# Kernel optimization log

Hardware: AMD Instinct MI355X
Metric: run time of the kernel (lower is better)

Reference implementation:

```python
import jax, jax.numpy as jnp
import numpy as np

B, N, D, H, DG = 1, 1024, 512, 8, 64
DK = D // H
EPS = 1e-5


def _layer_norm(x, g, b):
    m = jnp.mean(x, axis=-1, keepdims=True)
    v = jnp.var(x, axis=-1, keepdims=True)
    return (x - m) / jnp.sqrt(v + EPS) * g + b


def _box_rel_embedding(box):
    # box: (B, N, 4) = x_min, y_min, x_max, y_max
    x_min, y_min, x_max, y_max = [box[..., i] for i in range(4)]  # each (B, N)
    cx = (x_min + x_max) * 0.5
    cy = (y_min + y_max) * 0.5
    w = x_max - x_min + 1.0
    h = y_max - y_min + 1.0
    dx = jnp.log(jnp.clip(jnp.abs((cx[:, :, None] - cx[:, None, :]) / w[:, :, None]), 0.001))
    dy = jnp.log(jnp.clip(jnp.abs((cy[:, :, None] - cy[:, None, :]) / h[:, :, None]), 0.001))
    dw = jnp.log(w[:, :, None] / w[:, None, :])
    dh = jnp.log(h[:, :, None] / h[:, None, :])
    pos = jnp.stack([dx, dy, dw, dh], axis=-1)  # (B, N, N, 4)
    dim_mat = 1.0 / jnp.power(1000.0, jnp.arange(DG // 8, dtype=jnp.float32) / (DG // 8))  # (8,)
    mul = (100.0 * pos[..., None] * dim_mat).reshape(pos.shape[0], pos.shape[1], pos.shape[2], -1)  # (B,N,N,32)
    return jnp.concatenate([jnp.sin(mul), jnp.cos(mul)], axis=-1)  # (B, N, N, 64)


def _split_heads(x, W, b):
    # torch permute(2,0,1,3).view(-1, len, d_k): head-major flattening
    return (x @ W.T + b).reshape(B, N, H, DK).transpose(2, 0, 1, 3).reshape(H * B, N, DK)


def _forward(input_query, input_key, input_value, input_box,
             Wq, bq, Wk, bk, Wv, bv, Wo, bo, WG_w, WG_b,
             ln0_g, ln0_b, ln_g, ln_b):
    residual = input_query
    emb = _box_rel_embedding(input_box)  # (B, N, N, 64)
    # per-head linear (64 -> 1) then relu: (B, H, N, N)
    w_g = jax.nn.relu(jnp.einsum('bijg,hg->bhij', emb, WG_w) + WG_b[None, :, None, None])
    q = _split_heads(input_query, Wq, bq)  # (H*B, N, DK)
    k = _split_heads(input_key, Wk, bk)
    v = _split_heads(input_value, Wv, bv)
    scores = jnp.einsum('xnd,xmd->xnm', q, k) / np.sqrt(DK).astype(np.float32)  # (H*B, N, N)
    # original adds (B,H,N,N) to (H*B,N,N): only valid for B==1
    w_mn = jax.nn.softmax(jnp.log(jnp.clip(w_g.reshape(H * B, N, N), 1e-6)) + scores, axis=-1)
    x = jnp.einsum('xnm,xmd->xnd', w_mn, v)  # (H*B, N, DK)
    # faithful to original: transpose(1,2) then view(nbatches, -1, h*d_k)
    x = x.transpose(0, 2, 1).reshape(B, -1, H * DK)  # (B, N, D)
    out0 = _layer_norm(x + residual, ln0_g, ln0_b)
    out = out0 @ Wo.T + bo  # dropout = identity (eval mode)
    return _layer_norm(out + out0, ln_g, ln_b)


def setup_inputs() -> dict:
    key = jax.random.key(0)
    ks = jax.random.split(key, 12)
    inp = {}
    inp['input_query'] = jax.random.normal(ks[0], (B, N, D), dtype=jnp.float32)
    inp['input_key'] = jax.random.normal(ks[1], (B, N, D), dtype=jnp.float32)
    inp['input_value'] = jax.random.normal(ks[2], (B, N, D), dtype=jnp.float32)
    mins = jax.random.uniform(ks[3], (B, N, 2), dtype=jnp.float32) * 500.0
    sizes = jax.random.uniform(ks[4], (B, N, 2), dtype=jnp.float32) * 99.0 + 1.0
    inp['input_box'] = jnp.concatenate([mins, mins + sizes], axis=-1)  # valid boxes
    s = 0.02
    inp['Wq'] = jax.random.normal(ks[5], (D, D), dtype=jnp.float32) * s
    inp['bq'] = jnp.zeros((D,), dtype=jnp.float32)
    inp['Wk'] = jax.random.normal(ks[6], (D, D), dtype=jnp.float32) * s
    inp['bk'] = jnp.zeros((D,), dtype=jnp.float32)
    inp['Wv'] = jax.random.normal(ks[7], (D, D), dtype=jnp.float32) * s
    inp['bv'] = jnp.zeros((D,), dtype=jnp.float32)
    inp['Wo'] = jax.random.normal(ks[8], (D, D), dtype=jnp.float32) * s
    inp['bo'] = jnp.zeros((D,), dtype=jnp.float32)
    inp['WG_w'] = jax.random.normal(ks[9], (H, DG), dtype=jnp.float32) * 0.1
    inp['WG_b'] = jax.random.normal(ks[10], (H,), dtype=jnp.float32) * 0.1
    inp['ln0_g'] = jnp.ones((D,), dtype=jnp.float32)
    inp['ln0_b'] = jnp.zeros((D,), dtype=jnp.float32)
    inp['ln_g'] = jnp.ones((D,), dtype=jnp.float32)
    inp['ln_b'] = jnp.zeros((D,), dtype=jnp.float32)
    return inp


def reference(input_query, input_key, input_value, input_box,
              Wq, bq, Wk, bk, Wv, bv, Wo, bo, WG_w, WG_b,
              ln0_g, ln0_b, ln_g, ln_b):
    return _forward(input_query, input_key, input_value, input_box,
                    Wq, bq, Wk, bk, Wv, bv, Wo, bo, WG_w, WG_b,
                    ln0_g, ln0_b, ln_g, ln_b)
```

## Files before the change

kernel.cpp:

```cpp
#include <hip/hip_runtime.h>
#include <cstddef>

#define NTOK 1024
#define DMODEL 512
#define NHEAD 8
#define DKH 64
#define NSPLIT 8
#define JQ 128

typedef __attribute__((ext_vector_type(4))) float f32x4;
typedef __attribute__((ext_vector_type(8))) __bf16 bf16x8;
typedef __attribute__((ext_vector_type(4))) __bf16 bf16x4;
typedef __attribute__((ext_vector_type(4))) unsigned short u16x4;
typedef __attribute__((ext_vector_type(8))) unsigned short u16x8;
typedef __attribute__((ext_vector_type(4))) _Float16 f16x4;
typedef unsigned short ushort_t;

__device__ __forceinline__ float wave_sum_f(float v){
  #pragma unroll
  for (int m=1; m<64; m<<=1) v += __shfl_xor(v, m, 64);
  return v;
}
__device__ __forceinline__ unsigned short f2bf(float f){
  __bf16 b = (__bf16)f;
  return __builtin_bit_cast(unsigned short, b);
}
__device__ __forceinline__ float bf2f(unsigned short u){
  return (float)__builtin_bit_cast(__bf16, u);
}

__device__ __forceinline__ float fract_hw(float x){
  float r; asm("v_fract_f32 %0, %1" : "=v"(r) : "v"(x)); return r;
}
__device__ __forceinline__ float sin_rev(float rev){
  float f = fract_hw(rev);
  float s; asm("v_sin_f32 %0, %1" : "=v"(s) : "v"(f)); return s;
}
__device__ __forceinline__ float cos_rev(float rev){
  float f = fract_hw(rev);
  float c; asm("v_cos_f32 %0, %1" : "=v"(c) : "v"(f)); return c;
}
__device__ __forceinline__ float log_hw(float x){
  float l; asm("v_log_f32 %0, %1" : "=v"(l) : "v"(x));
  return 0.69314718056f * l;
}
__device__ __forceinline__ float exp_hw(float x){
  float y = x * 1.44269504f;
  float e; asm("v_exp_f32 %0, %1" : "=v"(e) : "v"(y));
  return e;
}

__global__ __launch_bounds__(256) void k_pre(
    const float* __restrict__ box, const float* __restrict__ WGw, const float* __restrict__ WGb,
    _Float16* __restrict__ wg16,
    const float* __restrict__ q, const float* __restrict__ k, const float* __restrict__ v,
    const float* __restrict__ wq, const float* __restrict__ wk, const float* __restrict__ wv,
    const float* __restrict__ wo,
    ushort_t* __restrict__ qb, ushort_t* __restrict__ kb, ushort_t* __restrict__ vb,
    ushort_t* __restrict__ wqb, ushort_t* __restrict__ wkb, ushort_t* __restrict__ wvb,
    ushort_t* __restrict__ wob){
  const int t = threadIdx.x;
  if (blockIdx.x >= 1024){
    int gi = (blockIdx.x - 1024)*256 + t;
    const float* s; ushort_t* d; int off;
    if (gi < 196608){
      int seg = gi >> 16;
      off = (gi & 65535)*8;
      s = seg==0 ? q : seg==1 ? k : v;
      d = seg==0 ? qb : seg==1 ? kb : vb;
    } else {
      int g2 = gi - 196608;
      int seg = g2 >> 15;
      off = (g2 & 32767)*8;
      s = seg==0 ? wq : seg==1 ? wk : seg==2 ? wv : wo;
      d = seg==0 ? wqb : seg==1 ? wkb : seg==2 ? wvb : wob;
    }
    float4 a = *(const float4*)(s + off);
    float4 b = *(const float4*)(s + off + 4);
    u16x4 o0, o1;
    o0[0]=f2bf(a.x); o0[1]=f2bf(a.y); o0[2]=f2bf(a.z); o0[3]=f2bf(a.w);
    o1[0]=f2bf(b.x); o1[1]=f2bf(b.y); o1[2]=f2bf(b.z); o1[3]=f2bf(b.w);
    *(u16x4*)(d + off) = o0;
    *(u16x4*)(d + off + 4) = o1;
    return;
  }
  __shared__ float arr[4][1024];
  #pragma unroll
  for (int u=0; u<4; u++){
    int idx = u*256 + t;
    float4 b4 = *(const float4*)(box + idx*4);
    arr[0][idx] = (b4.x + b4.z)*0.5f;
    arr[1][idx] = (b4.y + b4.w)*0.5f;
    arr[2][idx] = log_hw(b4.z - b4.x + 1.0f);
    arr[3][idx] = log_hw(b4.w - b4.y + 1.0f);
  }
  const int i = blockIdx.x;
  const int lane = t & 63, w = t >> 6, li = lane & 15, g = lane >> 4;
  float4 bi = *(const float4*)(box + i*4);
  float wi = bi.z - bi.x + 1.0f, hi = bi.w - bi.y + 1.0f;
  float Pi = (g==0) ? (bi.x+bi.z)*0.5f : (g==1) ? (bi.y+bi.w)*0.5f
           : (g==2) ? log_hw(wi) : log_hw(hi);
  float Ri = (g==0) ? 1.0f/wi : (g==1) ? 1.0f/hi : 1.0f;
  const bool doLog = (g < 2);
  bf16x8 wfs = {}, wfc = {};
  float wgb_li = 0.0f;
  if (li < 8){
    #pragma unroll
    for (int e=0; e<8; e++){
      wfs[e] = (__bf16)WGw[li*64 + g*8 + e];
      wfc[e] = (__bf16)WGw[li*64 + 32 + g*8 + e];
    }
    wgb_li = WGb[li];
  }
  __syncthreads();
  const float* parr = &arr[g][0];
  const float DMrev[8] = {15.9154943f, 6.7115094f, 2.8302196f, 1.1934938f,
                          0.5032921f, 0.2122365f, 0.08949941f, 0.0377416f};
  const int jbeg = w*256;
  for (int it=0; it<16; ++it){
    int j = jbeg + it*16 + li;
    float diff = (Pi - parr[j])*Ri;
    float lg = log_hw(fmaxf(fabsf(diff), 1e-3f));
    float dv = doLog ? lg : diff;
    bf16x8 afs, afc;
    #pragma unroll
    for (int e=0; e<8; e++){
      float rev = dv * DMrev[e];
      afs[e] = (__bf16)sin_rev(rev);
      afc[e] = (__bf16)cos_rev(rev);
    }
    f32x4 acc = (f32x4){0.f,0.f,0.f,0.f};
    acc = __builtin_amdgcn_mfma_f32_16x16x32_bf16(afs, wfs, acc, 0,0,0);
    acc = __builtin_amdgcn_mfma_f32_16x16x32_bf16(afc, wfc, acc, 0,0,0);
    if (li < 8){
      f16x4 o;
      #pragma unroll
      for (int r=0; r<4; r++)
        o[r] = (_Float16)fmaxf(acc[r] + wgb_li, 6.103515625e-05f);
      *(f16x4*)(wg16 + (((size_t)li<<20) + ((size_t)i<<10) + jbeg + it*16 + g*4)) = o;
    }
  }
}

__global__ __launch_bounds__(128) void k_mm_qkv(
    const ushort_t* __restrict__ Aq, const ushort_t* __restrict__ Ak, const ushort_t* __restrict__ Av,
    const ushort_t* __restrict__ Wqb, const ushort_t* __restrict__ Wkb, const ushort_t* __restrict__ Wvb,
    const float* __restrict__ bq, const float* __restrict__ bk, const float* __restrict__ bv,
    ushort_t* __restrict__ Qb, ushort_t* __restrict__ Kb, ushort_t* __restrict__ Vt){
  const int z = blockIdx.z;
  const ushort_t* A = z==0 ? Aq : z==1 ? Ak : Av;
  const ushort_t* W = z==0 ? Wqb : z==1 ? Wkb : Wvb;
  const float* bias = z==0 ? bq : z==1 ? bk : bv;
  const int t = threadIdx.x, lane = t & 63, w = t >> 6;
  const int li = lane & 15, g = lane >> 4;
  const int m0 = blockIdx.y*32;
  const int n0 = blockIdx.x*64 + w*32;
  const ushort_t* ar = A + (size_t)(m0+li)*DMODEL + g*8;
  const ushort_t* wr = W + (size_t)(n0+li)*DMODEL + g*8;
  f32x4 acc[2][2] = {};
  if (z < 2){
    #pragma unroll
    for (int k0=0; k0<DMODEL; k0+=64){
      bf16x8 wf0a = *(const bf16x8*)(wr + k0);
      bf16x8 wf0b = *(const bf16x8*)(wr + k0 + 32);
      bf16x8 wf1a = *(const bf16x8*)(wr + 16*DMODEL + k0);
      bf16x8 wf1b = *(const bf16x8*)(wr + 16*DMODEL + k0 + 32);
      bf16x8 af0a = *(const bf16x8*)(ar + k0);
      bf16x8 af0b = *(const bf16x8*)(ar + k0 + 32);
      bf16x8 af1a = *(const bf16x8*)(ar + 16*DMODEL + k0);
      bf16x8 af1b = *(const bf16x8*)(ar + 16*DMODEL + k0 + 32);
      acc[0][0] = __builtin_amdgcn_mfma_f32_16x16x32_bf16(wf0a, af0a, acc[0][0], 0,0,0);
      acc[0][0] = __builtin_amdgcn_mfma_f32_16x16x32_bf16(wf0b, af0b, acc[0][0], 0,0,0);
      acc[0][1] = __builtin_amdgcn_mfma_f32_16x16x32_bf16(wf0a, af1a, acc[0][1], 0,0,0);
      acc[0][1] = __builtin_amdgcn_mfma_f32_16x16x32_bf16(wf0b, af1b, acc[0][1], 0,0,0);
      acc[1][0] = __builtin_amdgcn_mfma_f32_16x16x32_bf16(wf1a, af0a, acc[1][0], 0,0,0);
      acc[1][0] = __builtin_amdgcn_mfma_f32_16x16x32_bf16(wf1b, af0b, acc[1][0], 0,0,0);
      acc[1][1] = __builtin_amdgcn_mfma_f32_16x16x32_bf16(wf1a, af1a, acc[1][1], 0,0,0);
      acc[1][1] = __builtin_amdgcn_mfma_f32_16x16x32_bf16(wf1b, af1b, acc[1][1], 0,0,0);
    }
    ushort_t* C = z ? Kb : Qb;
    #pragma unroll
    for (int nf=0; nf<2; nf++){
      int n = n0 + nf*16 + g*4;
      float4 b4 = *(const float4*)(bias + n);
      const float* bp = (const float*)&b4;
      #pragma unroll
      for (int mf=0; mf<2; mf++){
        int m = m0 + mf*16 + li;
        u16x4 o;
        #pragma unroll
        for (int r=0; r<4; r++) o[r] = f2bf(acc[nf][mf][r] + bp[r]);
        *(u16x4*)(C + (size_t)m*DMODEL + n) = o;
      }
    }
  } else {
    #pragma unroll
    for (int k0=0; k0<DMODEL; k0+=64){
      bf16x8 wf0a = *(const bf16x8*)(wr + k0);
      bf16x8 wf0b = *(const bf16x8*)(wr + k0 + 32);
      bf16x8 wf1a = *(const bf16x8*)(wr + 16*DMODEL + k0);
      bf16x8 wf1b = *(const bf16x8*)(wr + 16*DMODEL + k0 + 32);
      bf16x8 af0a = *(const bf16x8*)(ar + k0);
      bf16x8 af0b = *(const bf16x8*)(ar + k0 + 32);
      bf16x8 af1a = *(const bf16x8*)(ar + 16*DMODEL + k0);
      bf16x8 af1b = *(const bf16x8*)(ar + 16*DMODEL + k0 + 32);
      acc[0][0] = __builtin_amdgcn_mfma_f32_16x16x32_bf16(af0a, wf0a, acc[0][0], 0,0,0);
      acc[0][0] = __builtin_amdgcn_mfma_f32_16x16x32_bf16(af0b, wf0b, acc[0][0], 0,0,0);
      acc[0][1] = __builtin_amdgcn_mfma_f32_16x16x32_bf16(af0a, wf1a, acc[0][1], 0,0,0);
      acc[0][1] = __builtin_amdgcn_mfma_f32_16x16x32_bf16(af0b, wf1b, acc[0][1], 0,0,0);
      acc[1][0] = __builtin_amdgcn_mfma_f32_16x16x32_bf16(af1a, wf0a, acc[1][0], 0,0,0);
      acc[1][0] = __builtin_amdgcn_mfma_f32_16x16x32_bf16(af1b, wf0b, acc[1][0], 0,0,0);
      acc[1][1] = __builtin_amdgcn_mfma_f32_16x16x32_bf16(af1a, wf1a, acc[1][1], 0,0,0);
      acc[1][1] = __builtin_amdgcn_mfma_f32_16x16x32_bf16(af1b, wf1b, acc[1][1], 0,0,0);
    }
    #pragma unroll
    for (int mf=0; mf<2; mf++){
      int m = m0 + mf*16 + g*4;
      #pragma unroll
      for (int nf=0; nf<2; nf++){
        int n = n0 + nf*16 + li;
        float bn = bias[n];
        u16x4 o;
        #pragma unroll
        for (int r=0; r<4; r++) o[r] = f2bf(acc[mf][nf][r] + bn);
        *(u16x4*)(Vt + (((size_t)(n>>6))<<16) + ((size_t)(n&63)<<10) + m) = o;
      }
    }
  }
}

__global__ __launch_bounds__(512) void k_attn4(const ushort_t* __restrict__ Qb,
     const ushort_t* __restrict__ Kb, const ushort_t* __restrict__ Vt,
     const _Float16* __restrict__ wg, ushort_t* __restrict__ Xpt, float* __restrict__ rsp){
  __shared__ __align__(16) char smem[34816];
  ushort_t* Ks = (ushort_t*)smem;
  ushort_t* Vs = (ushort_t*)(smem + 17408);
  const int t = threadIdx.x;
  const int itg = blockIdx.x, h = blockIdx.y, sp = blockIdx.z;
  const int jbeg = sp*JQ;
  {
    const int r = t >> 3, c = (t & 7)*8;
    #pragma unroll
    for (int p=0; p<2; p++){
      u16x8 kv = *(const u16x8*)(Kb + (size_t)(jbeg + p*64 + r)*DMODEL + h*DKH + c);
      *(u16x8*)(Ks + (p*64 + r)*68 + c) = kv;
      u16x8 vv = *(const u16x8*)(Vt + ((size_t)h<<16) + (size_t)r*NTOK + jbeg + p*64 + c);
      *(u16x8*)(Vs + r*136 + p*64 + c) = vv;
    }
  }
  const int lane = t & 63, w = t >> 6;
  const int i0 = (itg*8 + w)*16;
  const int li = lane & 15, g = lane >> 4;
  const ushort_t* qp = Qb + (size_t)(i0+li)*DMODEL + h*DKH + g*8;
  bf16x8 qf0 = *(const bf16x8*)(qp);
  bf16x8 qf1 = *(const bf16x8*)(qp + 32);
  const _Float16* gbase = wg + ((size_t)h<<20) + ((size_t)(i0+li)<<10) + jbeg + g*4;
  f32x4 xacc[4];
  #pragma unroll
  for (int mf=0; mf<4; mf++) xacc[mf] = (f32x4){0.f,0.f,0.f,0.f};
  float rsum = 0.f;
  __syncthreads();
  #pragma unroll
  for (int jj = 0; jj < JQ; jj += 32){
    const ushort_t* kp = Ks + (jj + li)*68 + g*8;
    bf16x8 a00 = *(const bf16x8*)(kp);
    bf16x8 a01 = *(const bf16x8*)(kp + 32);
    bf16x8 a10 = *(const bf16x8*)(kp + 16*68);
    bf16x8 a11 = *(const bf16x8*)(kp + 16*68 + 32);
    f32x4 s0 = (f32x4){0.f,0.f,0.f,0.f};
    f32x4 s1 = (f32x4){0.f,0.f,0.f,0.f};
    s0 = __builtin_amdgcn_mfma_f32_16x16x32_bf16(a00, qf0, s0, 0,0,0);
    s0 = __builtin_amdgcn_mfma_f32_16x16x32_bf16(a01, qf1, s0, 0,0,0);
    s1 = __builtin_amdgcn_mfma_f32_16x16x32_bf16(a10, qf0, s1, 0,0,0);
    s1 = __builtin_amdgcn_mfma_f32_16x16x32_bf16(a11, qf1, s1, 0,0,0);
    f16x4 g0 = *(const f16x4*)(gbase + jj);
    f16x4 g1 = *(const f16x4*)(gbase + jj + 16);
    float p[8];
    #pragma unroll
    for (int r=0; r<4; r++){ p[r]   = (float)g0[r] * exp_hw(s0[r]*0.125f); rsum += p[r]; }
    #pragma unroll
    for (int r=0; r<4; r++){ p[4+r] = (float)g1[r] * exp_hw(s1[r]*0.125f); rsum += p[4+r]; }
    bf16x8 pb;
    pb[0]=(__bf16)p[0]; pb[1]=(__bf16)p[1]; pb[2]=(__bf16)p[2]; pb[3]=(__bf16)p[3];
    pb[4]=(__bf16)p[4]; pb[5]=(__bf16)p[5]; pb[6]=(__bf16)p[6]; pb[7]=(__bf16)p[7];
    #pragma unroll
    for (int mf=0; mf<4; mf++){
      const ushort_t* vp = Vs + (size_t)(li + mf*16)*136 + jj + g*4;
      bf16x4 lo = *(const bf16x4*)(vp);
      bf16x4 hi = *(const bf16x4*)(vp + 16);
      bf16x8 vf = __builtin_shufflevector(lo, hi, 0,1,2,3,4,5,6,7);
      xacc[mf] = __builtin_amdgcn_mfma_f32_16x16x32_bf16(vf, pb, xacc[mf], 0,0,0);
    }
  }
  rsum += __shfl_xor(rsum, 16, 64);
  rsum += __shfl_xor(rsum, 32, 64);
  if (lane < 16) rsp[((size_t)sp*NHEAD + h)*NTOK + i0 + li] = rsum;
  __syncthreads();
  float* xw = (float*)smem + w*(16*68);
  #pragma unroll
  for (int mf=0; mf<4; mf++)
    *(f32x4*)&xw[li*68 + mf*16 + g*4] = xacc[mf];
  __builtin_amdgcn_s_waitcnt(0);
  float xv[16];
  #pragma unroll
  for (int r=0; r<16; r++) xv[r] = xw[r*68 + lane];
  u16x8 o0, o1;
  #pragma unroll
  for (int r=0; r<8; r++){ o0[r] = f2bf(xv[r]); o1[r] = f2bf(xv[8+r]); }
  ushort_t* xp = Xpt + (((size_t)sp*NHEAD + h)*DKH + lane)*NTOK + i0;
  *(u16x8*)(xp)     = o0;
  *(u16x8*)(xp + 8) = o1;
}

__global__ __launch_bounds__(256) void k_ln0c(const ushort_t* __restrict__ Xpt,
        const float* __restrict__ rsp, const float* __restrict__ resid,
        const float* __restrict__ g, const float* __restrict__ b,
        float* __restrict__ out0, ushort_t* __restrict__ out0b){
  const int n = blockIdx.x, t = threadIdx.x;
  const int h = n >> 7, dk = (n >> 1) & 63, mo = (n & 1)*512;
  const int i0 = mo + t, i1 = mo + t + 256;
  float s0v=0.f, s1v=0.f, r0=0.f, r1=0.f;
  #pragma unroll
  for (int sp=0; sp<NSPLIT; sp++){
    const ushort_t* base = Xpt + (((size_t)sp*NHEAD + h)*DKH + dk)*NTOK;
    s0v += bf2f(base[i0]);
    s1v += bf2f(base[i1]);
    const float* rb = rsp + ((size_t)sp*NHEAD + h)*NTOK;
    r0 += rb[i0];
    r1 += rb[i1];
  }
  float x0 = s0v/r0 + resid[(size_t)n*DMODEL + t];
  float x1 = s1v/r1 + resid[(size_t)n*DMODEL + t + 256];
  __shared__ float red[8];
  float s = wave_sum_f(x0 + x1);
  float q = wave_sum_f(x0*x0 + x1*x1);
  int wid = t >> 6, lane = t & 63;
  if (lane == 0){ red[wid] = s; red[4+wid] = q; }
  __syncthreads();
  float S = red[0]+red[1]+red[2]+red[3];
  float Q = red[4]+red[5]+red[6]+red[7];
  float mean = S * (1.0f/512.0f);
  float var = Q * (1.0f/512.0f) - mean*mean;
  float rs = rsqrtf(var + 1e-5f);
  float y0 = (x0-mean)*rs*g[t] + b[t];
  float y1 = (x1-mean)*rs*g[t+256] + b[t+256];
  out0[(size_t)n*DMODEL + t]        = y0;
  out0[(size_t)n*DMODEL + t + 256]  = y1;
  out0b[(size_t)n*DMODEL + t]       = f2bf(y0);
  out0b[(size_t)n*DMODEL + t + 256] = f2bf(y1);
}

__global__ __launch_bounds__(512) void k_mm_o_ln(
    const ushort_t* __restrict__ A, const ushort_t* __restrict__ W,
    const float* __restrict__ bo, const float* __restrict__ add,
    const float* __restrict__ lng, const float* __restrict__ lnb, float* __restrict__ out){
  const int t = threadIdx.x, lane = t & 63, w = t >> 6;
  const int li = lane & 15, g = lane >> 4;
  const int m0 = blockIdx.x*16;
  const int n0 = w*64;
  const ushort_t* ar = A + (size_t)(m0+li)*DMODEL + g*8;
  const ushort_t* wr = W + (size_t)(n0+li)*DMODEL + g*8;
  f32x4 acc[4] = {};
  #pragma unroll
  for (int k0=0; k0<DMODEL; k0+=64){
    bf16x8 afa = *(const bf16x8*)(ar + k0);
    bf16x8 afb = *(const bf16x8*)(ar + k0 + 32);
    #pragma unroll
    for (int nf=0; nf<4; nf++){
      const ushort_t* wp = wr + (size_t)nf*16*DMODEL + k0;
      bf16x8 wfa = *(const bf16x8*)(wp);
      bf16x8 wfb = *(const bf16x8*)(wp + 32);
      acc[nf] = __builtin_amdgcn_mfma_f32_16x16x32_bf16(wfa, afa, acc[nf], 0,0,0);
      acc[nf] = __builtin_amdgcn_mfma_f32_16x16x32_bf16(wfb, afb, acc[nf], 0,0,0);
    }
  }
  const int m = m0 + li;
  float s = 0.f, qq = 0.f;
  f32x4 v[4];
  #pragma unroll
  for (int nf=0; nf<4; nf++){
    int n = n0 + nf*16 + g*4;
    f32x4 b4 = *(const f32x4*)(bo + n);
    f32x4 a4 = *(const f32x4*)(add + (size_t)m*DMODEL + n);
    #pragma unroll
    for (int r=0; r<4; r++){
      float x = acc[nf][r] + b4[r] + a4[r];
      v[nf][r] = x; s += x; qq += x*x;
    }
  }
  s  += __shfl_xor(s, 16, 64);  s  += __shfl_xor(s, 32, 64);
  qq += __shfl_xor(qq, 16, 64); qq += __shfl_xor(qq, 32, 64);
  __shared__ float red[8][16][2];
  if (g == 0){ red[w][li][0] = s; red[w][li][1] = qq; }
  __syncthreads();
  float S = 0.f, Q = 0.f;
  #pragma unroll
  for (int u=0; u<8; u++){ S += red[u][li][0]; Q += red[u][li][1]; }
  float mean = S * (1.0f/512.0f);
  float var = Q * (1.0f/512.0f) - mean*mean;
  float rs = rsqrtf(var + 1e-5f);
  #pragma unroll
  for (int nf=0; nf<4; nf++){
    int n = n0 + nf*16 + g*4;
    f32x4 g4 = *(const f32x4*)(lng + n);
    f32x4 be = *(const f32x4*)(lnb + n);
    f32x4 o;
    #pragma unroll
    for (int r=0; r<4; r++) o[r] = (v[nf][r]-mean)*rs*g4[r] + be[r];
    *(f32x4*)(out + (size_t)m*DMODEL + n) = o;
  }
}

extern "C" void kernel_launch(void* const* d_in, const int* in_sizes, int n_in,
                              void* d_out, int out_size, void* d_ws, size_t ws_size,
                              hipStream_t stream){
  (void)in_sizes; (void)n_in; (void)out_size; (void)ws_size;
  const float* in_q = (const float*)d_in[0];
  const float* in_k = (const float*)d_in[1];
  const float* in_v = (const float*)d_in[2];
  const float* box  = (const float*)d_in[3];
  const float* Wq   = (const float*)d_in[4];
  const float* bq   = (const float*)d_in[5];
  const float* Wk   = (const float*)d_in[6];
  const float* bk   = (const float*)d_in[7];
  const float* Wv   = (const float*)d_in[8];
  const float* bv   = (const float*)d_in[9];
  const float* Wo   = (const float*)d_in[10];
  const float* bo   = (const float*)d_in[11];
  const float* WGw  = (const float*)d_in[12];
  const float* WGb  = (const float*)d_in[13];
  const float* ln0g = (const float*)d_in[14];
  const float* ln0b = (const float*)d_in[15];
  const float* lng  = (const float*)d_in[16];
  const float* lnb  = (const float*)d_in[17];

  float* ws = (float*)d_ws;
  ushort_t* Abq  = (ushort_t*)(ws + 0);
  ushort_t* Abk  = (ushort_t*)(ws + 262144);
  ushort_t* Abv  = (ushort_t*)(ws + 524288);
  ushort_t* Wqb  = (ushort_t*)(ws + 786432);
  ushort_t* Wkb  = (ushort_t*)(ws + 917504);
  ushort_t* Wvb  = (ushort_t*)(ws + 1048576);
  ushort_t* Wob  = (ushort_t*)(ws + 1179648);
  ushort_t* Qb   = (ushort_t*)(ws + 1310720);
  ushort_t* Kb   = (ushort_t*)(ws + 1572864);
  ushort_t* Vt   = (ushort_t*)(ws + 1835008);
  _Float16* wg16 = (_Float16*)(ws + 2097152);
  ushort_t* Xpt  = (ushort_t*)(ws + 6291456);
  float*    rsp  = ws + 8388608;
  float*    out0 = ws + 8454144;
  ushort_t* out0b= (ushort_t*)(ws + 8978432);
  float*    out  = (float*)d_out;

  k_pre<<<dim3(2304), dim3(256), 0, stream>>>(box, WGw, WGb, wg16,
            in_q, in_k, in_v, Wq, Wk, Wv, Wo,
            Abq, Abk, Abv, Wqb, Wkb, Wvb, Wob);
  k_mm_qkv<<<dim3(8,32,3), dim3(128), 0, stream>>>(Abq, Abk, Abv, Wqb, Wkb, Wvb,
            bq, bk, bv, Qb, Kb, Vt);
  k_attn4<<<dim3(8,8,8), dim3(512), 0, stream>>>(Qb, Kb, Vt, wg16, Xpt, rsp);
  k_ln0c<<<dim3(1024), dim3(256), 0, stream>>>(Xpt, rsp, in_q, ln0g, ln0b, out0, out0b);
  k_mm_o_ln<<<dim3(64), dim3(512), 0, stream>>>(out0b, Wob, bo, out0, lng, lnb, out);
}
```

Measured before the change: 78.38 us.

## Fuse QKV projection with fp32-to-bf16 conversion into front kernel

The separate bf16 conversion pass for inputs and weights and the standalone QKV GEMM kernel are merged into one front kernel. Extra blocks now load fp32 activations and weights, convert them to bf16 into LDS tiles and run the MFMA GEMM there, next to the box-embedding blocks and the Wo conversion. This removes one launch and the global round trip of the bf16 copies of q/k/v and the three weights, and lets the GEMM overlap with the geometry work. The cost is that each GEMM block reconverts shared weight and activation data redundantly and adds LDS staging with barriers.

```diff
diff --git a/kernel.cpp b/kernel.cpp
--- a/kernel.cpp
+++ b/kernel.cpp
@@ -50,52 +50,128 @@
   return e;
 }
 
-__global__ __launch_bounds__(256) void k_pre(
+__global__ __launch_bounds__(256) void k_front2(
     const float* __restrict__ box, const float* __restrict__ WGw, const float* __restrict__ WGb,
     _Float16* __restrict__ wg16,
-    const float* __restrict__ q, const float* __restrict__ k, const float* __restrict__ v,
-    const float* __restrict__ wq, const float* __restrict__ wk, const float* __restrict__ wv,
-    const float* __restrict__ wo,
-    ushort_t* __restrict__ qb, ushort_t* __restrict__ kb, ushort_t* __restrict__ vb,
-    ushort_t* __restrict__ wqb, ushort_t* __restrict__ wkb, ushort_t* __restrict__ wvb,
-    ushort_t* __restrict__ wob){
+    const float* __restrict__ inq, const float* __restrict__ ink, const float* __restrict__ inv,
+    const float* __restrict__ Wq, const float* __restrict__ Wk, const float* __restrict__ Wv,
+    const float* __restrict__ Wo,
+    const float* __restrict__ bq, const float* __restrict__ bk, const float* __restrict__ bv,
+    ushort_t* __restrict__ Qb, ushort_t* __restrict__ Kb, ushort_t* __restrict__ Vt,
+    ushort_t* __restrict__ Wob){
+  __shared__ __align__(16) char smem[17408];
   const int t = threadIdx.x;
-  if (blockIdx.x >= 1024){
-    int gi = (blockIdx.x - 1024)*256 + t;
-    const float* s; ushort_t* d; int off;
-    if (gi < 196608){
-      int seg = gi >> 16;
-      off = (gi & 65535)*8;
-      s = seg==0 ? q : seg==1 ? k : v;
-      d = seg==0 ? qb : seg==1 ? kb : vb;
-    } else {
-      int g2 = gi - 196608;
-      int seg = g2 >> 15;
-      off = (g2 & 32767)*8;
-      s = seg==0 ? wq : seg==1 ? wk : seg==2 ? wv : wo;
-      d = seg==0 ? wqb : seg==1 ? wkb : seg==2 ? wvb : wob;
-    }
-    float4 a = *(const float4*)(s + off);
-    float4 b = *(const float4*)(s + off + 4);
+  const int lane = t & 63, w = t >> 6, li = lane & 15, g = lane >> 4;
+  if (blockIdx.x >= 1408){
+    int off = ((blockIdx.x - 1408)*256 + t)*8;
+    float4 a = *(const float4*)(Wo + off);
+    float4 b4 = *(const float4*)(Wo + off + 4);
     u16x4 o0, o1;
     o0[0]=f2bf(a.x); o0[1]=f2bf(a.y); o0[2]=f2bf(a.z); o0[3]=f2bf(a.w);
-    o1[0]=f2bf(b.x); o1[1]=f2bf(b.y); o1[2]=f2bf(b.z); o1[3]=f2bf(b.w);
-    *(u16x4*)(d + off) = o0;
-    *(u16x4*)(d + off + 4) = o1;
+    o1[0]=f2bf(b4.x); o1[1]=f2bf(b4.y); o1[2]=f2bf(b4.z); o1[3]=f2bf(b4.w);
+    *(u16x4*)(Wob + off) = o0;
+    *(u16x4*)(Wob + off + 4) = o1;
     return;
   }
-  __shared__ float arr[4][1024];
-  #pragma unroll
-  for (int u=0; u<4; u++){
-    int idx = u*256 + t;
+  if (blockIdx.x >= 1024){
+    const int u = blockIdx.x - 1024;
+    const int z = u >> 7;
+    const int rem = u & 127;
+    const int m0 = (rem >> 3)*64;
+    const int n0 = (rem & 7)*64;
+    const float* A = z==0 ? inq : z==1 ? ink : inv;
+    const float* W = z==0 ? Wq : z==1 ? Wk : Wv;
+    const float* bias = z==0 ? bq : z==1 ? bk : bv;
+    ushort_t* Al = (ushort_t*)smem;
+    ushort_t* Wl = (ushort_t*)(smem + 8704);
+    const int row = t >> 2, kq = (t & 3)*16;
+    const int mrb = (w >> 1)*32;
+    const int nrb = (w & 1)*32;
+    f32x4 acc[2][2] = {};
+    for (int k0 = 0; k0 < DMODEL; k0 += 64){
+      {
+        const float* ap = A + (size_t)(m0+row)*DMODEL + k0 + kq;
+        const float* wp = W + (size_t)(n0+row)*DMODEL + k0 + kq;
+        #pragma unroll
+        for (int q=0; q<4; q++){
+          float4 av = *(const float4*)(ap + q*4);
+          float4 wv = *(const float4*)(wp + q*4);
+          u16x4 pa, pw;
+          pa[0]=f2bf(av.x); pa[1]=f2bf(av.y); pa[2]=f2bf(av.z); pa[3]=f2bf(av.w);
+          pw[0]=f2bf(wv.x); pw[1]=f2bf(wv.y); pw[2]=f2bf(wv.z); pw[3]=f2bf(wv.w);
+          *(u16x4*)(Al + row*68 + kq + q*4) = pa;
+          *(u16x4*)(Wl + row*68 + kq + q*4) = pw;
+        }
+      }
+      __syncthreads();
+      #pragma unroll
+      for (int kc=0; kc<64; kc+=32){
+        const ushort_t* arl = Al + (mrb + li)*68 + kc + g*8;
+        const ushort_t* wrl = Wl + (nrb + li)*68 + kc + g*8;
+        bf16x8 af0 = *(const bf16x8*)(arl);
+        bf16x8 af1 = *(const bf16x8*)(arl + 16*68);
+        bf16x8 wf0 = *(const bf16x8*)(wrl);
+        bf16x8 wf1 = *(const bf16x8*)(wrl + 16*68);
+        if (z < 2){
+          acc[0][0] = __builtin_amdgcn_mfma_f32_16x16x32_bf16(wf0, af0, acc[0][0], 0,0,0);
+          acc[0][1] = __builtin_amdgcn_mfma_f32_16x16x32_bf16(wf0, af1, acc[0][1], 0,0,0);
+          acc[1][0] = __builtin_amdgcn_mfma_f32_16x16x32_bf16(wf1, af0, acc[1][0], 0,0,0);
+          acc[1][1] = __builtin_amdgcn_mfma_f32_16x16x32_bf16(wf1, af1, acc[1][1], 0,0,0);
+        } else {
+          acc[0][0] = __builtin_amdgcn_mfma_f32_16x16x32_bf16(af0, wf0, acc[0][0], 0,0,0);
+          acc[0][1] = __builtin_amdgcn_mfma_f32_16x16x32_bf16(af0, wf1, acc[0][1], 0,0,0);
+          acc[1][0] = __builtin_amdgcn_mfma_f32_16x16x32_bf16(af1, wf0, acc[1][0], 0,0,0);
+          acc[1][1] = __builtin_amdgcn_mfma_f32_16x16x32_bf16(af1, wf1, acc[1][1], 0,0,0);
+        }
+      }
+      __syncthreads();
+    }
+    if (z < 2){
+      ushort_t* C = z ? Kb : Qb;
+      #pragma unroll
+      for (int nf=0; nf<2; nf++){
+        int n = n0 + nrb + nf*16 + g*4;
+        float4 b4 = *(const float4*)(bias + n);
+        const float* bp = (const float*)&b4;
+        #pragma unroll
+        for (int mf=0; mf<2; mf++){
+          int m = m0 + mrb + mf*16 + li;
+          u16x4 o;
+          #pragma unroll
+          for (int r=0; r<4; r++) o[r] = f2bf(acc[nf][mf][r] + bp[r]);
+          *(u16x4*)(C + (size_t)m*DMODEL + n) = o;
+        }
+      }
+    } else {
+      #pragma unroll
+      for (int mf=0; mf<2; mf++){
+        int m = m0 + mrb + mf*16 + g*4;
+        #pragma unroll
+        for (int nf=0; nf<2; nf++){
+          int n = n0 + nrb + nf*16 + li;
+          float bn = bias[n];
+          u16x4 o;
+          #pragma unroll
+          for (int r=0; r<4; r++) o[r] = f2bf(acc[mf][nf][r] + bn);
+          *(u16x4*)(Vt + (((size_t)(n>>6))<<16) + ((size_t)(n&63)<<10) + m) = o;
+        }
+      }
+    }
+    return;
+  }
+  float* arr = (float*)smem;
+  {
+  }
+  #pragma unroll
+  for (int u2=0; u2<4; u2++){
+    int idx = u2*256 + t;
     float4 b4 = *(const float4*)(box + idx*4);
-    arr[0][idx] = (b4.x + b4.z)*0.5f;
-    arr[1][idx] = (b4.y + b4.w)*0.5f;
-    arr[2][idx] = log_hw(b4.z - b4.x + 1.0f);
-    arr[3][idx] = log_hw(b4.w - b4.y + 1.0f);
+    arr[idx]        = (b4.x + b4.z)*0.5f;
+    arr[1024+idx]   = (b4.y + b4.w)*0.5f;
+    arr[2048+idx]   = log_hw(b4.z - b4.x + 1.0f);
+    arr[3072+idx]   = log_hw(b4.w - b4.y + 1.0f);
   }
   const int i = blockIdx.x;
-  const int lane = t & 63, w = t >> 6, li = lane & 15, g = lane >> 4;
   float4 bi = *(const float4*)(box + i*4);
   float wi = bi.z - bi.x + 1.0f, hi = bi.w - bi.y + 1.0f;
   float Pi = (g==0) ? (bi.x+bi.z)*0.5f : (g==1) ? (bi.y+bi.w)*0.5f
@@ -113,7 +189,7 @@
     wgb_li = WGb[li];
   }
   __syncthreads();
-  const float* parr = &arr[g][0];
+  const float* parr = arr + g*1024;
   const float DMrev[8] = {15.9154943f, 6.7115094f, 2.8302196f, 1.1934938f,
                           0.5032921f, 0.2122365f, 0.08949941f, 0.0377416f};
   const int jbeg = w*256;
@@ -138,93 +214,6 @@
       for (int r=0; r<4; r++)
         o[r] = (_Float16)fmaxf(acc[r] + wgb_li, 6.103515625e-05f);
       *(f16x4*)(wg16 + (((size_t)li<<20) + ((size_t)i<<10) + jbeg + it*16 + g*4)) = o;
-    }
-  }
-}
-
-__global__ __launch_bounds__(128) void k_mm_qkv(
-    const ushort_t* __restrict__ Aq, const ushort_t* __restrict__ Ak, const ushort_t* __restrict__ Av,
-    const ushort_t* __restrict__ Wqb, const ushort_t* __restrict__ Wkb, const ushort_t* __restrict__ Wvb,
-    const float* __restrict__ bq, const float* __restrict__ bk, const float* __restrict__ bv,
-    ushort_t* __restrict__ Qb, ushort_t* __restrict__ Kb, ushort_t* __restrict__ Vt){
-  const int z = blockIdx.z;
-  const ushort_t* A = z==0 ? Aq : z==1 ? Ak : Av;
-  const ushort_t* W = z==0 ? Wqb : z==1 ? Wkb : Wvb;
-  const float* bias = z==0 ? bq : z==1 ? bk : bv;
-  const int t = threadIdx.x, lane = t & 63, w = t >> 6;
-  const int li = lane & 15, g = lane >> 4;
-  const int m0 = blockIdx.y*32;
-  const int n0 = blockIdx.x*64 + w*32;
-  const ushort_t* ar = A + (size_t)(m0+li)*DMODEL + g*8;
-  const ushort_t* wr = W + (size_t)(n0+li)*DMODEL + g*8;
-  f32x4 acc[2][2] = {};
-  if (z < 2){
-    #pragma unroll
-    for (int k0=0; k0<DMODEL; k0+=64){
-      bf16x8 wf0a = *(const bf16x8*)(wr + k0);
-      bf16x8 wf0b = *(const bf16x8*)(wr + k0 + 32);
-      bf16x8 wf1a = *(const bf16x8*)(wr + 16*DMODEL + k0);
-      bf16x8 wf1b = *(const bf16x8*)(wr + 16*DMODEL + k0 + 32);
-      bf16x8 af0a = *(const bf16x8*)(ar + k0);
-      bf16x8 af0b = *(const bf16x8*)(ar + k0 + 32);
-      bf16x8 af1a = *(const bf16x8*)(ar + 16*DMODEL + k0);
-      bf16x8 af1b = *(const bf16x8*)(ar + 16*DMODEL + k0 + 32);
-      acc[0][0] = __builtin_amdgcn_mfma_f32_16x16x32_bf16(wf0a, af0a, acc[0][0], 0,0,0);
-      acc[0][0] = __builtin_amdgcn_mfma_f32_16x16x32_bf16(wf0b, af0b, acc[0][0], 0,0,0);
-      acc[0][1] = __builtin_amdgcn_mfma_f32_16x16x32_bf16(wf0a, af1a, acc[0][1], 0,0,0);
-      acc[0][1] = __builtin_amdgcn_mfma_f32_16x16x32_bf16(wf0b, af1b, acc[0][1], 0,0,0);
-      acc[1][0] = __builtin_amdgcn_mfma_f32_16x16x32_bf16(wf1a, af0a, acc[1][0], 0,0,0);
-      acc[1][0] = __builtin_amdgcn_mfma_f32_16x16x32_bf16(wf1b, af0b, acc[1][0], 0,0,0);
-      acc[1][1] = __builtin_amdgcn_mfma_f32_16x16x32_bf16(wf1a, af1a, acc[1][1], 0,0,0);
-      acc[1][1] = __builtin_amdgcn_mfma_f32_16x16x32_bf16(wf1b, af1b, acc[1][1], 0,0,0);
-    }
-    ushort_t* C = z ? Kb : Qb;
-    #pragma unroll
-    for (int nf=0; nf<2; nf++){
-      int n = n0 + nf*16 + g*4;
-      float4 b4 = *(const float4*)(bias + n);
-      const float* bp = (const float*)&b4;
-      #pragma unroll
-      for (int mf=0; mf<2; mf++){
-        int m = m0 + mf*16 + li;
-        u16x4 o;
-        #pragma unroll
-        for (int r=0; r<4; r++) o[r] = f2bf(acc[nf][mf][r] + bp[r]);
-        *(u16x4*)(C + (size_t)m*DMODEL + n) = o;
-      }
-    }
-  } else {
-    #pragma unroll
-    for (int k0=0; k0<DMODEL; k0+=64){
-      bf16x8 wf0a = *(const bf16x8*)(wr + k0);
-      bf16x8 wf0b = *(const bf16x8*)(wr + k0 + 32);
-      bf16x8 wf1a = *(const bf16x8*)(wr + 16*DMODEL + k0);
-      bf16x8 wf1b = *(const bf16x8*)(wr + 16*DMODEL + k0 + 32);
-      bf16x8 af0a = *(const bf16x8*)(ar + k0);
-      bf16x8 af0b = *(const bf16x8*)(ar + k0 + 32);
-      bf16x8 af1a = *(const bf16x8*)(ar + 16*DMODEL + k0);
-      bf16x8 af1b = *(const bf16x8*)(ar + 16*DMODEL + k0 + 32);
-      acc[0][0] = __builtin_amdgcn_mfma_f32_16x16x32_bf16(af0a, wf0a, acc[0][0], 0,0,0);
-      acc[0][0] = __builtin_amdgcn_mfma_f32_16x16x32_bf16(af0b, wf0b, acc[0][0], 0,0,0);
-      acc[0][1] = __builtin_amdgcn_mfma_f32_16x16x32_bf16(af0a, wf1a, acc[0][1], 0,0,0);
-      acc[0][1] = __builtin_amdgcn_mfma_f32_16x16x32_bf16(af0b, wf1b, acc[0][1], 0,0,0);
-      acc[1][0] = __builtin_amdgcn_mfma_f32_16x16x32_bf16(af1a, wf0a, acc[1][0], 0,0,0);
-      acc[1][0] = __builtin_amdgcn_mfma_f32_16x16x32_bf16(af1b, wf0b, acc[1][0], 0,0,0);
-      acc[1][1] = __builtin_amdgcn_mfma_f32_16x16x32_bf16(af1a, wf1a, acc[1][1], 0,0,0);
-      acc[1][1] = __builtin_amdgcn_mfma_f32_16x16x32_bf16(af1b, wf1b, acc[1][1], 0,0,0);
-    }
-    #pragma unroll
-    for (int mf=0; mf<2; mf++){
-      int m = m0 + mf*16 + g*4;
-      #pragma unroll
-      for (int nf=0; nf<2; nf++){
-        int n = n0 + nf*16 + li;
-        float bn = bias[n];
-        u16x4 o;
-        #pragma unroll
-        for (int r=0; r<4; r++) o[r] = f2bf(acc[mf][nf][r] + bn);
-        *(u16x4*)(Vt + (((size_t)(n>>6))<<16) + ((size_t)(n&63)<<10) + m) = o;
-      }
     }
   }
 }
@@ -435,28 +424,19 @@
   const float* lnb  = (const float*)d_in[17];
 
   float* ws = (float*)d_ws;
-  ushort_t* Abq  = (ushort_t*)(ws + 0);
-  ushort_t* Abk  = (ushort_t*)(ws + 262144);
-  ushort_t* Abv  = (ushort_t*)(ws + 524288);
-  ushort_t* Wqb  = (ushort_t*)(ws + 786432);
-  ushort_t* Wkb  = (ushort_t*)(ws + 917504);
-  ushort_t* Wvb  = (ushort_t*)(ws + 1048576);
-  ushort_t* Wob  = (ushort_t*)(ws + 1179648);
-  ushort_t* Qb   = (ushort_t*)(ws + 1310720);
-  ushort_t* Kb   = (ushort_t*)(ws + 1572864);
-  ushort_t* Vt   = (ushort_t*)(ws + 1835008);
-  _Float16* wg16 = (_Float16*)(ws + 2097152);
-  ushort_t* Xpt  = (ushort_t*)(ws + 6291456);
-  float*    rsp  = ws + 8388608;
-  float*    out0 = ws + 8454144;
-  ushort_t* out0b= (ushort_t*)(ws + 8978432);
+  ushort_t* Wob  = (ushort_t*)(ws + 0);
+  ushort_t* Qb   = (ushort_t*)(ws + 131072);
+  ushort_t* Kb   = (ushort_t*)(ws + 393216);
+  ushort_t* Vt   = (ushort_t*)(ws + 655360);
+  _Float16* wg16 = (_Float16*)(ws + 917504);
+  ushort_t* Xpt  = (ushort_t*)(ws + 5111808);
+  float*    rsp  = ws + 7208960;
+  float*    out0 = ws + 7274496;
+  ushort_t* out0b= (ushort_t*)(ws + 7798784);
   float*    out  = (float*)d_out;
 
-  k_pre<<<dim3(2304), dim3(256), 0, stream>>>(box, WGw, WGb, wg16,
-            in_q, in_k, in_v, Wq, Wk, Wv, Wo,
-            Abq, Abk, Abv, Wqb, Wkb, Wvb, Wob);
-  k_mm_qkv<<<dim3(8,32,3), dim3(128), 0, stream>>>(Abq, Abk, Abv, Wqb, Wkb, Wvb,
-            bq, bk, bv, Qb, Kb, Vt);
+  k_front2<<<dim3(1536), dim3(256), 0, stream>>>(box, WGw, WGb, wg16,
+            in_q, in_k, in_v, Wq, Wk, Wv, Wo, bq, bk, bv, Qb, Kb, Vt, Wob);
   k_attn4<<<dim3(8,8,8), dim3(512), 0, stream>>>(Qb, Kb, Vt, wg16, Xpt, rsp);
   k_ln0c<<<dim3(1024), dim3(256), 0, stream>>>(Xpt, rsp, in_q, ln0g, ln0b, out0, out0b);
   k_mm_o_ln<<<dim3(64), dim3(512), 0, stream>>>(out0b, Wob, bo, out0, lng, lnb, out);
```

After: 73.26 us. 6.5% less time.
